# Kernel optimization log

Hardware: AMD Instinct MI355X
Metric: run time of the kernel (lower is better)

Reference implementation:

```python
import jax, jax.numpy as jnp
import numpy as np

NC, ND, B, K = 10000, 1000000, 8192, 64
EMB = 16
CH_DENSE, DEV_DENSE = 16, 20
CAT_MAX = [100, 4, 50, 200, 500, 1000, 300]  # lang, plat, os, country, carrier, brand, plat_os
H1, H2, ATTN_H = 64, 64, 84
IN1 = CH_DENSE + EMB        # 32  (channel dense + channel_id emb)
IN2 = DEV_DENSE + 7 * EMB   # 132 (device dense + 7 cat embs)


def setup_inputs() -> dict:
    key = jax.random.key(0)
    ks = jax.random.split(key, 32)
    def nrm(k, shape, s=0.05):
        return jax.random.normal(k, shape, dtype=jnp.float32) * s
    inp = {}
    inp["channel_dense"] = nrm(ks[0], (NC, CH_DENSE), 1.0)
    inp["device_dense"] = nrm(ks[1], (ND, DEV_DENSE), 1.0)
    inp["channel_id_emb"] = nrm(ks[2], (NC, EMB))
    names = ["lang_emb", "plat_emb", "os_emb", "country_emb", "carrier_emb", "brand_emb", "plat_os_emb"]
    for i, (n, m) in enumerate(zip(names, CAT_MAX)):
        inp[n] = nrm(ks[3 + i], (m, EMB))
    inp["W_agg"] = nrm(ks[10], (IN2, H2));  inp["b_agg"] = jnp.zeros((H2,), jnp.float32)
    inp["W_self"] = nrm(ks[11], (IN1, H1)); inp["b_self"] = jnp.zeros((H1,), jnp.float32)
    inp["W_attn"] = nrm(ks[12], (H2 + IN1, ATTN_H)); inp["b_attn"] = jnp.zeros((ATTN_H,), jnp.float32)
    inp["W_attn2"] = nrm(ks[13], (ATTN_H, 1)); inp["b_attn2"] = jnp.zeros((1,), jnp.float32)
    inp["channel_ids"] = jax.random.randint(ks[14], (NC,), 0, NC)
    cat_cols = [jax.random.randint(ks[15 + i], (ND,), 0, m) for i, m in enumerate(CAT_MAX)]
    inp["device_cat"] = jnp.stack(cat_cols, axis=1)  # [ND, 7]
    inp["vertices"] = jax.random.randint(ks[22], (B,), 0, NC)
    inp["bot_neibrs"] = jax.random.randint(ks[23], (B, K), 0, ND)
    inp["normal_neibrs"] = jax.random.randint(ks[24], (B, K), 0, ND)
    inp["bot_counts"] = jax.random.randint(ks[25], (B,), 1, K + 1)
    inp["normal_counts"] = jax.random.randint(ks[26], (B,), 1, K + 1)
    return inp


def reference(channel_dense, device_dense, channel_id_emb, lang_emb, plat_emb, os_emb,
              country_emb, carrier_emb, brand_emb, plat_os_emb,
              W_agg, b_agg, W_self, b_self, W_attn, b_attn, W_attn2, b_attn2,
              channel_ids, device_cat, vertices, bot_neibrs, normal_neibrs,
              bot_counts, normal_counts):
    cat_tables = [lang_emb, plat_emb, os_emb, country_emb, carrier_emb, brand_emb, plat_os_emb]
    # channel self features: dense cols + channel_id embedding  -> [B, IN1]
    ch_v = jnp.concatenate([channel_dense[vertices],
                            channel_id_emb[channel_ids[vertices]]], axis=1)

    def agg(neibrs, counts):
        # gather neighbor device features, embed categoricals, masked mean, linear (Mean_agg)
        dense = device_dense[neibrs]                                   # [B, K, DEV_DENSE]
        cats = device_cat[neibrs]                                      # [B, K, 7]
        embs = jnp.concatenate([t[cats[..., i]] for i, t in enumerate(cat_tables)], axis=-1)
        feats = jnp.concatenate([dense, embs], axis=-1)                # [B, K, IN2]
        mask = (jnp.arange(K)[None, :] < counts[:, None]).astype(feats.dtype)
        mean = jnp.sum(feats * mask[..., None], axis=1) / jnp.maximum(counts, 1).astype(feats.dtype)[:, None]
        return mean @ W_agg + b_agg                                    # [B, H2]

    bots = agg(bot_neibrs, bot_counts)
    normal = agg(normal_neibrs, normal_counts)

    def score(h):
        # attention MLP on concat(aggregated feats, channel self feats)
        return jax.nn.relu(jnp.concatenate([h, ch_v], axis=1) @ W_attn + b_attn) @ W_attn2 + b_attn2

    a = jax.nn.softmax(jnp.concatenate([score(bots), score(normal)], axis=1), axis=1)  # [B, 2]
    gcn = a[:, 0:1] * bots + a[:, 1:2] * normal                        # convex combination [B, H2]
    # Msg_out: relu(concat(agg_out, linear(self)))
    return jax.nn.relu(jnp.concatenate([gcn, ch_v @ W_self + b_self], axis=1))  # [B, H2+H1]
```

## Files before the change

### kernel.cpp

```cpp
#include <hip/hip_runtime.h>

#define BATCH 8192
#define KNB   64
#define EMB   16
#define CHD   16
#define DVD   20
#define H1    64
#define H2    64
#define AH    84
#define IN1   32
#define IN2   132

#define RB 32
#define VB 16
#define NIT 8
#define NBLK (2 * BATCH / NIT)

__global__ __launch_bounds__(256) void gconv_gather(
    const float* __restrict__ device_dense,
    const float* __restrict__ t0, const float* __restrict__ t1,
    const float* __restrict__ t2, const float* __restrict__ t3,
    const float* __restrict__ t4, const float* __restrict__ t5,
    const float* __restrict__ t6,
    const int* __restrict__ device_cat,
    const int* __restrict__ bot_neibrs,
    const int* __restrict__ normal_neibrs,
    const int* __restrict__ bot_counts,
    const int* __restrict__ normal_counts,
    float* __restrict__ fsum_ws)
{
    const int blk  = blockIdx.x;
    const int t    = threadIdx.x;
    const int w    = t >> 6;
    const int L    = t & 63;
    const int kk   = L >> 5;
    const int slot = L & 31;

    __shared__ alignas(16) int   ofs[2][KNB][8];
    __shared__ alignas(16) float psum[4][IN2];
    __shared__ alignas(16) float plat_lds[64];
    __shared__ int scnt[2];

    if (t < 64) plat_lds[t] = t1[t];

    const float* P = device_dense;
    int sIdx = 0, c4v = slot * 4, fb = slot * 4;
    if (slot >= 5 && slot < 29) {
        const int e  = slot - 5;
        const int tb = e >> 2;
        c4v  = (e & 3) * 4;
        sIdx = (tb == 0) ? 1 : (tb + 2);
        fb   = 20 + 16 * ((tb == 0) ? 0 : tb + 1) + c4v;
        switch (tb) {
            case 0: P = t0; break;
            case 1: P = t2; break;
            case 2: P = t3; break;
            case 3: P = t4; break;
            case 4: P = t5; break;
            default: P = t6; break;
        }
    }
    const bool isPlat = (slot >= 29);
    const int  pcol   = (slot - 29) * 4;
    if (isPlat) fb = 36 + pcol;

    auto stage = [&](int it, int buf) {
        if (w != (it & 3)) return;
        const int b  = blk * NIT + it;
        const int v  = b >> 1;
        const bool nh = b & 1;
        int cnt = nh ? normal_counts[v] : bot_counts[v];
        cnt = cnt < 1 ? 1 : (cnt > KNB ? KNB : cnt);
        int n = 0;
        if (L < cnt) n = (nh ? normal_neibrs : bot_neibrs)[v * KNB + L];
        const long cb = (long)n * 7;
        const int4 cA = *(const int4*)(device_cat + cb);
        const int4 cB = *(const int4*)(device_cat + cb + 3);
        *(int4*)&ofs[buf][L][0] = make_int4(n * DVD, cA.x * EMB, cA.y * EMB, cA.z * EMB);
        *(int4*)&ofs[buf][L][4] = make_int4(cA.w * EMB, cB.y * EMB, cB.z * EMB, cB.w * EMB);
        if (L == 0) scnt[buf] = cnt;
    };

    stage(0, 0);
    __syncthreads();

    int buf = 0;
    for (int it = 0; it < NIT; ++it) {
        if (it + 1 < NIT) stage(it + 1, buf ^ 1);

        const int cnt = scnt[buf];
        float4 acc  = make_float4(0.f, 0.f, 0.f, 0.f);
        float4 accx = make_float4(0.f, 0.f, 0.f, 0.f);

        #pragma unroll
        for (int c0 = 0; c0 < 8; c0 += 4) {
            if (2 * w + 8 * c0 >= cnt) break;
            const int kb = 2 * w + kk;
            if (!isPlat) {
                int o[4];
                #pragma unroll
                for (int i = 0; i < 4; ++i)
                    o[i] = ofs[buf][kb + 8 * (c0 + i)][sIdx];
                __builtin_amdgcn_sched_barrier(0);
                float4 val[4];
                #pragma unroll
                for (int i = 0; i < 4; ++i)
                    val[i] = *(const float4*)(P + o[i] + c4v);
                __builtin_amdgcn_sched_barrier(0);
                #pragma unroll
                for (int i = 0; i < 4; ++i) {
                    const float m = (kb + 8 * (c0 + i) < cnt) ? 1.f : 0.f;
                    acc.x = fmaf(m, val[i].x, acc.x);
                    acc.y = fmaf(m, val[i].y, acc.y);
                    acc.z = fmaf(m, val[i].z, acc.z);
                    acc.w = fmaf(m, val[i].w, acc.w);
                }
            } else {
                #pragma unroll
                for (int i = 0; i < 4; ++i) {
                    const int k = kb + 8 * (c0 + i);
                    const int o = ofs[buf][k][2];
                    const float m = (k < cnt) ? 1.f : 0.f;
                    const float4 pv = *(const float4*)&plat_lds[o + pcol];
                    acc.x = fmaf(m, pv.x, acc.x);
                    acc.y = fmaf(m, pv.y, acc.y);
                    acc.z = fmaf(m, pv.z, acc.z);
                    acc.w = fmaf(m, pv.w, acc.w);
                    if (slot == 29) {
                        const float4 pw = *(const float4*)&plat_lds[o + 12];
                        accx.x = fmaf(m, pw.x, accx.x);
                        accx.y = fmaf(m, pw.y, accx.y);
                        accx.z = fmaf(m, pw.z, accx.z);
                        accx.w = fmaf(m, pw.w, accx.w);
                    }
                }
            }
        }

        acc.x += __shfl_xor(acc.x, 32, 64);
        acc.y += __shfl_xor(acc.y, 32, 64);
        acc.z += __shfl_xor(acc.z, 32, 64);
        acc.w += __shfl_xor(acc.w, 32, 64);
        accx.x += __shfl_xor(accx.x, 32, 64);
        accx.y += __shfl_xor(accx.y, 32, 64);
        accx.z += __shfl_xor(accx.z, 32, 64);
        accx.w += __shfl_xor(accx.w, 32, 64);

        if (L < 32) {
            *(float4*)&psum[w][fb] = acc;
            if (slot == 29) *(float4*)&psum[w][48] = accx;
        }
        __syncthreads();

        if (t < IN2 / 4) {
            const float4 p0 = *(const float4*)&psum[0][t * 4];
            const float4 p1 = *(const float4*)&psum[1][t * 4];
            const float4 p2 = *(const float4*)&psum[2][t * 4];
            const float4 p3 = *(const float4*)&psum[3][t * 4];
            const int b = blk * NIT + it;
            *(float4*)(fsum_ws + (size_t)b * IN2 + t * 4) =
                make_float4(p0.x + p1.x + p2.x + p3.x,
                            p0.y + p1.y + p2.y + p3.y,
                            p0.z + p1.z + p2.z + p3.z,
                            p0.w + p1.w + p2.w + p3.w);
        }
        __syncthreads();
        buf ^= 1;
    }
}

__global__ __launch_bounds__(256) void gconv_dense(
    const float* __restrict__ channel_dense,
    const float* __restrict__ channel_id_emb,
    const float* __restrict__ W_agg,  const float* __restrict__ b_agg,
    const float* __restrict__ W_self, const float* __restrict__ b_self,
    const float* __restrict__ W_attn, const float* __restrict__ b_attn,
    const float* __restrict__ W_attn2,
    const int* __restrict__ channel_ids,
    const int* __restrict__ vertices,
    const int* __restrict__ bot_counts,
    const int* __restrict__ normal_counts,
    const float* __restrict__ fsum_ws,
    float* __restrict__ out)
{
    const int blk = blockIdx.x;
    const int b0  = blk * RB;
    const int v0  = blk * VB;
    const int t   = threadIdx.x;

    __shared__ alignas(16) float fs[RB][IN2];
    __shared__ alignas(16) float chvs[VB][IN1];
    __shared__ alignas(16) float hs[RB][H2];
    __shared__ float u_lds[AH][RB + 1];
    __shared__ float sarr[RB];
    __shared__ float cinv[RB];

    for (int idx = t; idx < RB * IN2 / 4; idx += 256) {
        const float4 vv = *(const float4*)(fsum_ws + (size_t)b0 * IN2 + idx * 4);
        *(float4*)&((float*)fs)[idx * 4] = vv;
    }
    if (t < RB) {
        const int b = b0 + t;
        const int v = b >> 1;
        int c = (b & 1) ? normal_counts[v] : bot_counts[v];
        c = (c > KNB) ? KNB : ((c < 1) ? 1 : c);
        cinv[t] = 1.0f / (float)c;
    }
    if (t < 128) {
        const int vx = t >> 3, q = t & 7;
        const int vert = vertices[v0 + vx];
        const float* src = (q < 4)
            ? channel_dense  + (size_t)vert * CHD + q * 4
            : channel_id_emb + (size_t)channel_ids[vert] * EMB + (q - 4) * 4;
        *(float4*)&chvs[vx][q * 4] = *(const float4*)src;
    }
    __syncthreads();

    {
        const int w = t >> 6, lane = t & 63;
        const int r0 = w * 8;
        float acc[8] = {0.f, 0.f, 0.f, 0.f, 0.f, 0.f, 0.f, 0.f};
        #pragma unroll 4
        for (int f = 0; f < IN2; ++f) {
            const float wv = W_agg[f * H2 + lane];
            #pragma unroll
            for (int r = 0; r < 8; ++r)
                acc[r] = fmaf(fs[r0 + r][f], wv, acc[r]);
        }
        const float bb = b_agg[lane];
        #pragma unroll
        for (int r = 0; r < 8; ++r)
            hs[r0 + r][lane] = fmaf(acc[r], cinv[r0 + r], bb);
    }
    __syncthreads();

    if (t < 2 * AH) {
        const int rg = (t >= AH) ? 1 : 0;
        const int aa = t - AH * rg;
        const int r0 = rg * 16;
        float acc[16];
        #pragma unroll
        for (int r = 0; r < 16; ++r) acc[r] = 0.f;
        #pragma unroll 2
        for (int f = 0; f < H2; ++f) {
            const float wv = W_attn[f * AH + aa];
            #pragma unroll
            for (int r = 0; r < 16; ++r)
                acc[r] = fmaf(hs[r0 + r][f], wv, acc[r]);
        }
        #pragma unroll 2
        for (int f = 0; f < IN1; ++f) {
            const float wv = W_attn[(H2 + f) * AH + aa];
            #pragma unroll
            for (int r = 0; r < 16; ++r)
                acc[r] = fmaf(chvs[(r0 + r) >> 1][f], wv, acc[r]);
        }
        const float ba = b_attn[aa], w2 = W_attn2[aa];
        #pragma unroll
        for (int r = 0; r < 16; ++r)
            u_lds[aa][r0 + r] = fmaxf(acc[r] + ba, 0.f) * w2;
    }
    __syncthreads();

    if (t < RB) {
        float s = 0.f;
        #pragma unroll 4
        for (int aa = 0; aa < AH; ++aa) s += u_lds[aa][t];
        sarr[t] = s;
    }
    __syncthreads();

    {
        const int vl = t >> 4;
        const int c8 = (t & 15) * 8;
        const float s0 = sarr[2 * vl], s1 = sarr[2 * vl + 1];
        const float mm = fmaxf(s0, s1);
        const float e0 = __expf(s0 - mm), e1 = __expf(s1 - mm);
        const float rs = 1.0f / (e0 + e1);
        const float a0 = e0 * rs, a1 = e1 * rs;
        float o[8];
        if (c8 < H2) {
            #pragma unroll
            for (int c = 0; c < 8; ++c)
                o[c] = fmaxf(a0 * hs[2 * vl][c8 + c] + a1 * hs[2 * vl + 1][c8 + c], 0.f);
        } else {
            const int cs = c8 - H2;
            float accS[8];
            #pragma unroll
            for (int c = 0; c < 8; ++c) accS[c] = b_self[cs + c];
            #pragma unroll 4
            for (int f = 0; f < IN1; ++f) {
                const float xv = chvs[vl][f];
                const float4 wa = *(const float4*)(W_self + f * H1 + cs);
                const float4 wb = *(const float4*)(W_self + f * H1 + cs + 4);
                accS[0] = fmaf(xv, wa.x, accS[0]);
                accS[1] = fmaf(xv, wa.y, accS[1]);
                accS[2] = fmaf(xv, wa.z, accS[2]);
                accS[3] = fmaf(xv, wa.w, accS[3]);
                accS[4] = fmaf(xv, wb.x, accS[4]);
                accS[5] = fmaf(xv, wb.y, accS[5]);
                accS[6] = fmaf(xv, wb.z, accS[6]);
                accS[7] = fmaf(xv, wb.w, accS[7]);
            }
            #pragma unroll
            for (int c = 0; c < 8; ++c) o[c] = fmaxf(accS[c], 0.f);
        }
        float4* op = (float4*)(out + (size_t)(v0 + vl) * (H1 + H2) + c8);
        op[0] = make_float4(o[0], o[1], o[2], o[3]);
        op[1] = make_float4(o[4], o[5], o[6], o[7]);
    }
}

extern "C" void kernel_launch(void* const* d_in, const int* in_sizes, int n_in,
                              void* d_out, int out_size, void* d_ws, size_t ws_size,
                              hipStream_t stream) {
    const float* channel_dense  = (const float*)d_in[0];
    const float* device_dense   = (const float*)d_in[1];
    const float* channel_id_emb = (const float*)d_in[2];
    const float* lang_emb       = (const float*)d_in[3];
    const float* plat_emb       = (const float*)d_in[4];
    const float* os_emb         = (const float*)d_in[5];
    const float* country_emb    = (const float*)d_in[6];
    const float* carrier_emb    = (const float*)d_in[7];
    const float* brand_emb      = (const float*)d_in[8];
    const float* plat_os_emb    = (const float*)d_in[9];
    const float* W_agg          = (const float*)d_in[10];
    const float* b_agg          = (const float*)d_in[11];
    const float* W_self         = (const float*)d_in[12];
    const float* b_self         = (const float*)d_in[13];
    const float* W_attn         = (const float*)d_in[14];
    const float* b_attn         = (const float*)d_in[15];
    const float* W_attn2        = (const float*)d_in[16];
    const int* channel_ids   = (const int*)d_in[18];
    const int* device_cat    = (const int*)d_in[19];
    const int* vertices      = (const int*)d_in[20];
    const int* bot_neibrs    = (const int*)d_in[21];
    const int* normal_neibrs = (const int*)d_in[22];
    const int* bot_counts    = (const int*)d_in[23];
    const int* normal_counts = (const int*)d_in[24];

    float* fsum_ws = (float*)d_ws;
    float* out     = (float*)d_out;

    gconv_gather<<<dim3(NBLK), dim3(256), 0, stream>>>(
        device_dense, lang_emb, plat_emb, os_emb, country_emb, carrier_emb,
        brand_emb, plat_os_emb, device_cat, bot_neibrs, normal_neibrs,
        bot_counts, normal_counts, fsum_ws);

    gconv_dense<<<dim3(2 * BATCH / RB), dim3(256), 0, stream>>>(
        channel_dense, channel_id_emb, W_agg, b_agg, W_self, b_self,
        W_attn, b_attn, W_attn2, channel_ids, vertices,
        bot_counts, normal_counts, fsum_ws, out);
}
```

Baseline: 75.98 us.

## Preload neighbor indices, triple-buffer offset staging, and contiguous per-wave neighbor chunks

At block start, all neighbor indices and counts for the block's eight rows are loaded into LDS. The device_cat offset staging moves to a triple buffer that runs two iterations ahead on waves 2 and 3. Each wave now handles a contiguous chunk of 16 neighbors and issues 8 independent gathers per thread instead of two rounds of 4, which raises memory-level parallelism. The trade-offs are more LDS use, extra work for the staging waves, and an early-exit granularity based on 16-neighbor chunks.

Result: no change. 77.29 us (+1.7%).

```diff
diff --git a/kernel.cpp b/kernel.cpp
--- a/kernel.cpp
+++ b/kernel.cpp
@@ -36,12 +36,40 @@
     const int kk   = L >> 5;
     const int slot = L & 31;
 
-    __shared__ alignas(16) int   ofs[2][KNB][8];
+    __shared__ int nidx[NIT][KNB];
+    __shared__ int scnt[NIT];
+    __shared__ alignas(16) int   ofs[3][KNB][8];
     __shared__ alignas(16) float psum[4][IN2];
     __shared__ alignas(16) float plat_lds[64];
-    __shared__ int scnt[2];
 
     if (t < 64) plat_lds[t] = t1[t];
+    if (t < NIT) {
+        const int b = blk * NIT + t;
+        int c = (b & 1) ? normal_counts[b >> 1] : bot_counts[b >> 1];
+        scnt[t] = c < 1 ? 1 : (c > KNB ? KNB : c);
+    }
+    {
+        const int b0 = blk * NIT + w;
+        nidx[w][L] = ((b0 & 1) ? normal_neibrs : bot_neibrs)[(b0 >> 1) * KNB + L];
+        const int b1 = blk * NIT + w + 4;
+        nidx[w + 4][L] = ((b1 & 1) ? normal_neibrs : bot_neibrs)[(b1 >> 1) * KNB + L];
+    }
+    __syncthreads();
+
+    auto stage = [&](int it, int wv) {
+        if (w != wv) return;
+        const int n  = (L < scnt[it]) ? nidx[it][L] : 0;
+        const long cb = (long)n * 7;
+        const int4 cA = *(const int4*)(device_cat + cb);
+        const int4 cB = *(const int4*)(device_cat + cb + 3);
+        const int bb = it % 3;
+        *(int4*)&ofs[bb][L][0] = make_int4(n * DVD, cA.x * EMB, cA.y * EMB, cA.z * EMB);
+        *(int4*)&ofs[bb][L][4] = make_int4(cA.w * EMB, cB.y * EMB, cB.z * EMB, cB.w * EMB);
+    };
+
+    stage(0, 3);
+    stage(1, 2);
+    __syncthreads();
 
     const float* P = device_dense;
     int sIdx = 0, c4v = slot * 4, fb = slot * 4;
@@ -62,77 +90,51 @@
     }
     const bool isPlat = (slot >= 29);
     const int  pcol   = (slot - 29) * 4;
-    if (isPlat) fb = 36 + pcol;
-
-    auto stage = [&](int it, int buf) {
-        if (w != (it & 3)) return;
-        const int b  = blk * NIT + it;
-        const int v  = b >> 1;
-        const bool nh = b & 1;
-        int cnt = nh ? normal_counts[v] : bot_counts[v];
-        cnt = cnt < 1 ? 1 : (cnt > KNB ? KNB : cnt);
-        int n = 0;
-        if (L < cnt) n = (nh ? normal_neibrs : bot_neibrs)[v * KNB + L];
-        const long cb = (long)n * 7;
-        const int4 cA = *(const int4*)(device_cat + cb);
-        const int4 cB = *(const int4*)(device_cat + cb + 3);
-        *(int4*)&ofs[buf][L][0] = make_int4(n * DVD, cA.x * EMB, cA.y * EMB, cA.z * EMB);
-        *(int4*)&ofs[buf][L][4] = make_int4(cA.w * EMB, cB.y * EMB, cB.z * EMB, cB.w * EMB);
-        if (L == 0) scnt[buf] = cnt;
-    };
-
-    stage(0, 0);
-    __syncthreads();
-
-    int buf = 0;
+    if (isPlat) { sIdx = 2; fb = 36 + pcol; }
+
     for (int it = 0; it < NIT; ++it) {
-        if (it + 1 < NIT) stage(it + 1, buf ^ 1);
-
-        const int cnt = scnt[buf];
+        if (it + 2 < NIT) stage(it + 2, (it & 1) ? 2 : 3);
+
+        const int cnt = scnt[it];
+        const int buf = it % 3;
         float4 acc  = make_float4(0.f, 0.f, 0.f, 0.f);
         float4 accx = make_float4(0.f, 0.f, 0.f, 0.f);
 
-        #pragma unroll
-        for (int c0 = 0; c0 < 8; c0 += 4) {
-            if (2 * w + 8 * c0 >= cnt) break;
-            const int kb = 2 * w + kk;
+        if (16 * w < cnt) {
+            const int k0 = 16 * w + kk;
+            int o[8];
+            #pragma unroll
+            for (int j = 0; j < 8; ++j)
+                o[j] = ofs[buf][k0 + 2 * j][sIdx];
+            __builtin_amdgcn_sched_barrier(0);
+            float4 val[8];
             if (!isPlat) {
-                int o[4];
                 #pragma unroll
-                for (int i = 0; i < 4; ++i)
-                    o[i] = ofs[buf][kb + 8 * (c0 + i)][sIdx];
-                __builtin_amdgcn_sched_barrier(0);
-                float4 val[4];
-                #pragma unroll
-                for (int i = 0; i < 4; ++i)
-                    val[i] = *(const float4*)(P + o[i] + c4v);
-                __builtin_amdgcn_sched_barrier(0);
-                #pragma unroll
-                for (int i = 0; i < 4; ++i) {
-                    const float m = (kb + 8 * (c0 + i) < cnt) ? 1.f : 0.f;
-                    acc.x = fmaf(m, val[i].x, acc.x);
-                    acc.y = fmaf(m, val[i].y, acc.y);
-                    acc.z = fmaf(m, val[i].z, acc.z);
-                    acc.w = fmaf(m, val[i].w, acc.w);
-                }
+                for (int j = 0; j < 8; ++j)
+                    val[j] = *(const float4*)(P + o[j] + c4v);
             } else {
                 #pragma unroll
-                for (int i = 0; i < 4; ++i) {
-                    const int k = kb + 8 * (c0 + i);
-                    const int o = ofs[buf][k][2];
-                    const float m = (k < cnt) ? 1.f : 0.f;
-                    const float4 pv = *(const float4*)&plat_lds[o + pcol];
-                    acc.x = fmaf(m, pv.x, acc.x);
-                    acc.y = fmaf(m, pv.y, acc.y);
-                    acc.z = fmaf(m, pv.z, acc.z);
-                    acc.w = fmaf(m, pv.w, acc.w);
-                    if (slot == 29) {
-                        const float4 pw = *(const float4*)&plat_lds[o + 12];
-                        accx.x = fmaf(m, pw.x, accx.x);
-                        accx.y = fmaf(m, pw.y, accx.y);
-                        accx.z = fmaf(m, pw.z, accx.z);
-                        accx.w = fmaf(m, pw.w, accx.w);
-                    }
+                for (int j = 0; j < 8; ++j)
+                    val[j] = *(const float4*)&plat_lds[o[j] + pcol];
+            }
+            __builtin_amdgcn_sched_barrier(0);
+            #pragma unroll
+            for (int j = 0; j < 8; ++j) {
+                const float m = (k0 + 2 * j < cnt) ? 1.f : 0.f;
+                acc.x = fmaf(m, val[j].x, acc.x);
+                acc.y = fmaf(m, val[j].y, acc.y);
+                acc.z = fmaf(m, val[j].z, acc.z);
+                acc.w = fmaf(m, val[j].w, acc.w);
+            }
+            if (slot == 29) {
+                #pragma unroll
+                for (int j = 0; j < 8; ++j) {
+                    const float m = (k0 + 2 * j < cnt) ? 1.f : 0.f;
+                    const float4 pw = *(const float4*)&plat_lds[o[j] + 12];
+                    accx.x = fmaf(m, pw.x, accx.x);
+                    accx.y = fmaf(m, pw.y, accx.y);
+                    accx.z = fmaf(m, pw.z, accx.z);
+                    accx.w = fmaf(m, pw.w, accx.w);
                 }
             }
         }
@@ -152,7 +154,7 @@
         }
         __syncthreads();
 
-        if (t < IN2 / 4) {
+        if (t < 33) {
             const float4 p0 = *(const float4*)&psum[0][t * 4];
             const float4 p1 = *(const float4*)&psum[1][t * 4];
             const float4 p2 = *(const float4*)&psum[2][t * 4];
@@ -165,7 +167,6 @@
                             p0.w + p1.w + p2.w + p3.w);
         }
         __syncthreads();
-        buf ^= 1;
     }
 }
 
```
